# Performance work log

Measured on AMD Instinct MI355X. Metric: run time of the kernel, lower is better.

## Reference

```python
import jax, jax.numpy as jnp
import numpy as np
from jax import lax

B, S, H, T = 64, 512, 1024, 67


def setup_inputs() -> dict:
    key = jax.random.key(0)
    ks = jax.random.split(key, 8)
    hidden = jax.random.normal(ks[0], (B, S, H), jnp.float32)
    labels = jax.random.randint(ks[1], (B, S), 0, T)
    lengths = jax.random.randint(ks[2], (B,), S // 2, S + 1)
    mask = (jnp.arange(S)[None, :] < lengths[:, None]).astype(jnp.int32)  # prefix mask, mask[:,0]=1
    W = jax.random.normal(ks[3], (H, T), jnp.float32) * 0.02
    b = jnp.zeros((T,), jnp.float32)
    start_trans = jax.random.uniform(ks[4], (T,), jnp.float32, -0.1, 0.1)
    end_trans = jax.random.uniform(ks[5], (T,), jnp.float32, -0.1, 0.1)
    trans = jax.random.uniform(ks[6], (T, T), jnp.float32, -0.1, 0.1)
    return dict(hidden=hidden, labels=labels, mask=mask, W=W, b=b,
                start_trans=start_trans, end_trans=end_trans, trans=trans)


def _crf_llh(em, tags, mask, start_trans, end_trans, trans):
    # em: (B,S,T), tags: (B,S) int, mask: (B,S) bool. torchcrf log-likelihood per sequence.
    maskf = mask.astype(em.dtype)
    # numerator: score of the gold path
    em_tag = jnp.take_along_axis(em, tags[:, :, None], axis=2)[:, :, 0]       # (B,S)
    num = start_trans[tags[:, 0]] + em_tag[:, 0]
    trans_tag = trans[tags[:, :-1], tags[:, 1:]]                              # (B,S-1)
    num = num + jnp.sum((trans_tag + em_tag[:, 1:]) * maskf[:, 1:], axis=1)
    last_idx = jnp.sum(mask.astype(jnp.int32), axis=1) - 1                    # (B,)
    last_tags = jnp.take_along_axis(tags, last_idx[:, None], axis=1)[:, 0]
    num = num + end_trans[last_tags]
    # denominator: log partition via forward algorithm (scan over time)
    def step(score, x):
        em_i, m_i = x  # (B,T), (B,)
        nxt = jax.nn.logsumexp(score[:, :, None] + trans[None] + em_i[:, None, :], axis=1)
        return jnp.where(m_i[:, None], nxt, score), None
    init = start_trans[None, :] + em[:, 0]
    score, _ = lax.scan(step, init, (em[:, 1:].transpose(1, 0, 2), mask[:, 1:].T))
    denom = jax.nn.logsumexp(score + end_trans[None, :], axis=1)
    return num - denom


def _viterbi(em, mask, start_trans, end_trans, trans):
    # returns best tag sequence (B,S), padded positions set to 0
    n_tags = em.shape[-1]
    ident = jnp.arange(n_tags)[None, :]
    def fwd(score, x):
        em_i, m_i = x  # (B,T), (B,)
        cand = score[:, :, None] + trans[None]                                # (B,T,T)
        idx = jnp.argmax(cand, axis=1)                                        # (B,T)
        nxt = jnp.max(cand, axis=1) + em_i
        score = jnp.where(m_i[:, None], nxt, score)
        idx = jnp.where(m_i[:, None], idx, ident)  # identity link on padded steps
        return score, idx
    init = start_trans[None, :] + em[:, 0]
    score, hist = lax.scan(fwd, init, (em[:, 1:].transpose(1, 0, 2), mask[:, 1:].T))
    best = jnp.argmax(score + end_trans[None, :], axis=1)                     # (B,)
    def back(carry, h):  # carry = tag at t+1, h = hist[t]: (B,T)
        prev = jnp.take_along_axis(h, carry[:, None], axis=1)[:, 0]
        return prev, prev
    _, ys = lax.scan(back, best, hist, reverse=True)                          # (S-1,B) tags[0..S-2]
    tags = jnp.concatenate([ys.transpose(1, 0), best[:, None]], axis=1)       # (B,S)
    return jnp.where(mask, tags, 0)


def reference(hidden, labels, mask, W, b, start_trans, end_trans, trans):
    maskb = mask.astype(bool)
    # dropout is identity in eval mode
    em = jnp.einsum('bsh,ht->bst', jax.nn.leaky_relu(hidden, 0.01), W) + b     # token_scores
    llh = _crf_llh(em, labels, maskb, start_trans, end_trans, trans)
    loss = -jnp.sum(llh) / em.shape[0]
    tags = _viterbi(em, maskb, start_trans, end_trans, trans)
    return loss, tags, em
```

## Files before the change

kernel.cpp:

```cpp
#include <hip/hip_runtime.h>

#define Bn 64
#define Sn 512
#define Hn 1024
#define Tn 67

#define LOG2E 1.4426950408889634f
#define LN2   0.6931471805599453f

__global__ __launch_bounds__(256) void gemm_em(
    const float* __restrict__ hidden, const float* __restrict__ W,
    const float* __restrict__ bias, float* __restrict__ em,
    float* __restrict__ out)
{
    __shared__ __align__(16) float hs[64][36];
    __shared__ __align__(16) float wt[80][36];

    const int tid = threadIdx.x;
    const int tx = tid & 15, ty = tid >> 4;
    const int row0 = blockIdx.x * 64;

    if (blockIdx.x == 0 && tid == 0) out[0] = 0.0f;

    float acc[4][5];
#pragma unroll
    for (int u = 0; u < 4; ++u)
#pragma unroll
        for (int v = 0; v < 5; ++v) acc[u][v] = 0.f;

    for (int kc = 0; kc < Hn; kc += 32) {
#pragma unroll
        for (int l = 0; l < 2; ++l) {
            int idx = tid + l * 256;
            int r = idx >> 3, kq = (idx & 7) << 2;
            float4 v = *reinterpret_cast<const float4*>(
                &hidden[(size_t)(row0 + r) * Hn + kc + kq]);
            v.x = v.x > 0.f ? v.x : 0.01f * v.x;
            v.y = v.y > 0.f ? v.y : 0.01f * v.y;
            v.z = v.z > 0.f ? v.z : 0.01f * v.z;
            v.w = v.w > 0.f ? v.w : 0.01f * v.w;
            *reinterpret_cast<float4*>(&hs[r][kq]) = v;
        }
        for (int idx = tid; idx < 32 * Tn; idx += 256) {
            int k = idx / Tn;
            int t = idx - k * Tn;
            wt[t][k] = W[(size_t)(kc + k) * Tn + t];
        }
        __syncthreads();

#pragma unroll
        for (int k0 = 0; k0 < 32; k0 += 4) {
            float4 hv[4], wv[5];
#pragma unroll
            for (int u = 0; u < 4; ++u)
                hv[u] = *reinterpret_cast<float4*>(&hs[ty + 16 * u][k0]);
#pragma unroll
            for (int v = 0; v < 5; ++v)
                wv[v] = *reinterpret_cast<float4*>(&wt[tx + 16 * v][k0]);
#pragma unroll
            for (int u = 0; u < 4; ++u)
#pragma unroll
                for (int v = 0; v < 5; ++v) {
                    acc[u][v] = fmaf(hv[u].x, wv[v].x, acc[u][v]);
                    acc[u][v] = fmaf(hv[u].y, wv[v].y, acc[u][v]);
                    acc[u][v] = fmaf(hv[u].z, wv[v].z, acc[u][v]);
                    acc[u][v] = fmaf(hv[u].w, wv[v].w, acc[u][v]);
                }
        }
        __syncthreads();
    }

#pragma unroll
    for (int v = 0; v < 5; ++v) {
        int c = tx + 16 * v;
        if (c < Tn) {
            float bb = bias[c];
#pragma unroll
            for (int u = 0; u < 4; ++u) {
                int row = row0 + ty + 16 * u;
                em[(size_t)row * Tn + c] = acc[u][v] + bb;
            }
        }
    }
}

__global__ __launch_bounds__(128) void crf_scan(
    const float* __restrict__ em, const int* __restrict__ labels,
    const int* __restrict__ mask, const float* __restrict__ startT,
    const float* __restrict__ endT, const float* __restrict__ trans,
    float* __restrict__ out)
{
    __shared__ __align__(16) float sArr[68];
    __shared__ __align__(16) float pArr[68];
    __shared__ float redf[128];
    __shared__ int   redi[128];
    __shared__ unsigned char hist[Sn - 1][68];
    __shared__ int tg[Sn];

    const int tid = threadIdx.x;
    const bool isV = blockIdx.x >= 64;
    const int b = blockIdx.x & 63;
    const int j = tid;
    const bool act = j < Tn;
    const int jj = act ? j : 0;
    const float* emb = em + (size_t)b * Sn * Tn;
    const int* maskb = mask + b * Sn;

    if (tid == 67) { sArr[67] = -1e30f; pArr[67] = 0.f; }

    if (!isV) {
        float Ecol[68];
#pragma unroll
        for (int i = 0; i < Tn; ++i)
            Ecol[i] = exp2f(trans[i * Tn + jj] * LOG2E);
        Ecol[67] = 0.f;

        float sc = act ? (startT[jj] + emb[jj]) : -1e30f;
        if (act) sArr[j] = sc;
        __syncthreads();

        float em_cur = act ? emb[(size_t)Tn + jj] : 0.f;
        int m_cur = maskb[1];

        for (int t = 1; t < Sn; ++t) {
            float em_nxt = 0.f; int m_nxt = 0;
            if (t + 1 < Sn) {
                em_nxt = act ? emb[(size_t)(t + 1) * Tn + jj] : 0.f;
                m_nxt = maskb[t + 1];
            }
            float mx = -1e30f;
#pragma unroll
            for (int i4 = 0; i4 < 17; ++i4) {
                float4 v = *reinterpret_cast<float4*>(&sArr[4 * i4]);
                mx = fmaxf(mx, fmaxf(fmaxf(v.x, v.y), fmaxf(v.z, v.w)));
            }
            float p = act ? exp2f((sc - mx) * LOG2E) : 0.f;
            if (act) pArr[j] = p;
            __syncthreads();
            float a0 = 0.f, a1 = 0.f, a2 = 0.f, a3 = 0.f;
#pragma unroll
            for (int i4 = 0; i4 < 17; ++i4) {
                float4 pv = *reinterpret_cast<float4*>(&pArr[4 * i4]);
                a0 = fmaf(pv.x, Ecol[4 * i4 + 0], a0);
                a1 = fmaf(pv.y, Ecol[4 * i4 + 1], a1);
                a2 = fmaf(pv.z, Ecol[4 * i4 + 2], a2);
                a3 = fmaf(pv.w, Ecol[4 * i4 + 3], a3);
            }
            float ssum = (a0 + a1) + (a2 + a3);
            float nxt = mx + log2f(ssum) * LN2 + em_cur;
            if (m_cur) sc = nxt;
            if (act) sArr[j] = sc;
            __syncthreads();
            em_cur = em_nxt; m_cur = m_nxt;
        }

        float v = act ? (sc + endT[jj]) : -1e30f;
        if (act) sArr[j] = v;
        __syncthreads();
        float mx = -1e30f;
#pragma unroll
        for (int i4 = 0; i4 < 17; ++i4) {
            float4 sv = *reinterpret_cast<float4*>(&sArr[4 * i4]);
            mx = fmaxf(mx, fmaxf(fmaxf(sv.x, sv.y), fmaxf(sv.z, sv.w)));
        }
        float p = act ? exp2f((v - mx) * LOG2E) : 0.f;
        if (act) pArr[j] = p;
        __syncthreads();
        float s0 = 0.f;
#pragma unroll
        for (int i4 = 0; i4 < 17; ++i4) {
            float4 pv = *reinterpret_cast<float4*>(&pArr[4 * i4]);
            s0 += (pv.x + pv.y) + (pv.z + pv.w);
        }
        float denom = mx + log2f(s0) * LN2;

        float part = 0.f; int lenp = 0;
        for (int s = tid; s < Sn; s += 128) {
            int ms = maskb[s];
            lenp += ms;
            int ls = labels[b * Sn + s];
            if (s == 0) {
                part += startT[ls] + emb[ls];
            } else if (ms) {
                int lp = labels[b * Sn + s - 1];
                part += trans[lp * Tn + ls] + emb[(size_t)s * Tn + ls];
            }
        }
        redf[tid] = part; redi[tid] = lenp;
        __syncthreads();
        if (tid == 0) {
            float num = 0.f; int len = 0;
            for (int i = 0; i < 128; ++i) { num += redf[i]; len += redi[i]; }
            int last = labels[b * Sn + len - 1];
            num += endT[last];
            float llh = num - denom;
            atomicAdd(out, -llh * (1.0f / (float)Bn));
        }
    } else {
        float Tcol[68];
#pragma unroll
        for (int i = 0; i < Tn; ++i) Tcol[i] = trans[i * Tn + jj];
        Tcol[67] = 0.f;

        float sc = act ? (startT[jj] + emb[jj]) : -1e30f;
        if (act) sArr[j] = sc;
        __syncthreads();

        float em_cur = act ? emb[(size_t)Tn + jj] : 0.f;
        int m_cur = maskb[1];

        for (int t = 1; t < Sn; ++t) {
            float em_nxt = 0.f; int m_nxt = 0;
            if (t + 1 < Sn) {
                em_nxt = act ? emb[(size_t)(t + 1) * Tn + jj] : 0.f;
                m_nxt = maskb[t + 1];
            }
            float best = -1e30f; int bi = 0;
#pragma unroll
            for (int i4 = 0; i4 < 17; ++i4) {
                float4 sv = *reinterpret_cast<float4*>(&sArr[4 * i4]);
                float c0 = sv.x + Tcol[4 * i4 + 0];
                if (c0 > best) { best = c0; bi = 4 * i4 + 0; }
                float c1 = sv.y + Tcol[4 * i4 + 1];
                if (c1 > best) { best = c1; bi = 4 * i4 + 1; }
                float c2 = sv.z + Tcol[4 * i4 + 2];
                if (c2 > best) { best = c2; bi = 4 * i4 + 2; }
                float c3 = sv.w + Tcol[4 * i4 + 3];
                if (c3 > best) { best = c3; bi = 4 * i4 + 3; }
            }
            float nxt = best + em_cur;
            int idx = m_cur ? bi : j;
            if (m_cur) sc = nxt;
            __syncthreads();
            if (act) { hist[t - 1][j] = (unsigned char)idx; sArr[j] = sc; }
            __syncthreads();
            em_cur = em_nxt; m_cur = m_nxt;
        }

        float v = act ? (sc + endT[jj]) : -1e30f;
        if (act) pArr[j] = v;
        __syncthreads();
        if (tid == 0) {
            float best = -1e30f; int bi = 0;
            for (int i = 0; i < Tn; ++i) {
                float c = pArr[i];
                if (c > best) { best = c; bi = i; }
            }
            int carry = bi;
            tg[Sn - 1] = carry;
            for (int k = Sn - 2; k >= 0; --k) {
                carry = hist[k][carry];
                tg[k] = carry;
            }
        }
        __syncthreads();
        float* tagsOut = out + 1 + b * Sn;
        for (int s = tid; s < Sn; s += 128)
            tagsOut[s] = maskb[s] ? (float)tg[s] : 0.f;
    }
}

extern "C" void kernel_launch(void* const* d_in, const int* in_sizes, int n_in,
                              void* d_out, int out_size, void* d_ws, size_t ws_size,
                              hipStream_t stream) {
    const float* hidden = (const float*)d_in[0];
    const int*   labels = (const int*)d_in[1];
    const int*   maskp  = (const int*)d_in[2];
    const float* W      = (const float*)d_in[3];
    const float* bias   = (const float*)d_in[4];
    const float* startT = (const float*)d_in[5];
    const float* endT   = (const float*)d_in[6];
    const float* trans  = (const float*)d_in[7];
    float* out = (float*)d_out;
    float* em  = out + 1 + (size_t)Bn * Sn;

    hipLaunchKernelGGL(gemm_em, dim3((Bn * Sn) / 64), dim3(256), 0, stream,
                       hidden, W, bias, em, out);
    hipLaunchKernelGGL(crf_scan, dim3(128), dim3(128), 0, stream,
                       em, labels, maskp, startT, endT, trans, out);
}
```

Baseline: 849.2 us.

## Fuse CRF forward and Viterbi into one block, staging emissions in LDS

Forward and Viterbi scans for a batch row now run in one 256-thread block, two waves each, instead of separate blocks. Emissions are double-buffered in shared memory in 32-step chunks so the serial loop avoids global loads. The forward pass shifts by the previous step's tag-0 score instead of recomputing a max, which drops one barrier per step. Viterbi uses a tree argmax. Risks: the stale shift could lose numerical stability, and each branch calls its own barrier inside the loop, relying on matching counts across divergent waves.

```diff
diff --git a/kernel.cpp b/kernel.cpp
--- a/kernel.cpp
+++ b/kernel.cpp
@@ -84,180 +84,211 @@
     }
 }
 
-__global__ __launch_bounds__(128) void crf_scan(
+__global__ __launch_bounds__(256) void crf_scan2(
     const float* __restrict__ em, const int* __restrict__ labels,
     const int* __restrict__ mask, const float* __restrict__ startT,
     const float* __restrict__ endT, const float* __restrict__ trans,
     float* __restrict__ out)
 {
-    __shared__ __align__(16) float sArr[68];
-    __shared__ __align__(16) float pArr[68];
-    __shared__ float redf[128];
-    __shared__ int   redi[128];
+    __shared__ __align__(16) float pbuf[2][72];
+    __shared__ __align__(16) float vbuf[2][72];
+    __shared__ __align__(16) float em_lds[2][32 * Tn];
+    __shared__ int mask_lds[Sn];
     __shared__ unsigned char hist[Sn - 1][68];
     __shared__ int tg[Sn];
+    __shared__ float redf[256];
+    __shared__ int redi[256];
 
     const int tid = threadIdx.x;
-    const bool isV = blockIdx.x >= 64;
-    const int b = blockIdx.x & 63;
-    const int j = tid;
-    const bool act = j < Tn;
-    const int jj = act ? j : 0;
-    const float* emb = em + (size_t)b * Sn * Tn;
-    const int* maskb = mask + b * Sn;
-
-    if (tid == 67) { sArr[67] = -1e30f; pArr[67] = 0.f; }
-
-    if (!isV) {
+    const int wid = tid >> 6;
+    const int lane = tid & 63;
+    const int b = blockIdx.x;
+    const bool isCRF = wid < 2;
+    const bool hiw = (wid & 1);
+    const int st = hiw ? (64 + (lane < 3 ? lane : 2)) : lane;
+    const bool active = (!hiw) || (lane < 3);
+    const float* emg = em + (size_t)b * Sn * Tn;
+
+    for (int i = tid; i < 32 * Tn; i += 256) em_lds[0][i] = emg[i];
+    for (int i = tid; i < Sn; i += 256) mask_lds[i] = mask[b * Sn + i];
+    if (tid == 0) {
+        pbuf[0][67] = 0.f; pbuf[1][67] = 0.f;
+        vbuf[0][67] = -1e30f; vbuf[1][67] = -1e30f;
+    }
+    __syncthreads();
+
+    float sc = startT[st] + em_lds[0][st];
+    if (isCRF) { if (active) pbuf[1][st] = sc; }
+    else       { if (active) vbuf[0][st] = sc; }
+    __syncthreads();
+    if (isCRF) {
+        float M0 = pbuf[1][0];
+        float p = exp2f((sc - M0) * LOG2E);
+        if (active) pbuf[0][st] = p;
+        if (tid == 0) { pbuf[0][68] = sc; pbuf[0][69] = M0; }
+    }
+    __syncthreads();
+
+    int bufc = 0;
+    if (isCRF) {
         float Ecol[68];
 #pragma unroll
-        for (int i = 0; i < Tn; ++i)
-            Ecol[i] = exp2f(trans[i * Tn + jj] * LOG2E);
+        for (int i = 0; i < Tn; ++i) Ecol[i] = exp2f(trans[i * Tn + st] * LOG2E);
         Ecol[67] = 0.f;
 
-        float sc = act ? (startT[jj] + emb[jj]) : -1e30f;
-        if (act) sArr[j] = sc;
-        __syncthreads();
-
-        float em_cur = act ? emb[(size_t)Tn + jj] : 0.f;
-        int m_cur = maskb[1];
-
         for (int t = 1; t < Sn; ++t) {
-            float em_nxt = 0.f; int m_nxt = 0;
-            if (t + 1 < Sn) {
-                em_nxt = act ? emb[(size_t)(t + 1) * Tn + jj] : 0.f;
-                m_nxt = maskb[t + 1];
-            }
-            float mx = -1e30f;
-#pragma unroll
-            for (int i4 = 0; i4 < 17; ++i4) {
-                float4 v = *reinterpret_cast<float4*>(&sArr[4 * i4]);
-                mx = fmaxf(mx, fmaxf(fmaxf(v.x, v.y), fmaxf(v.z, v.w)));
-            }
-            float p = act ? exp2f((sc - mx) * LOG2E) : 0.f;
-            if (act) pArr[j] = p;
+            if ((t & 31) == 1) {
+                int k = (t >> 5) + 1;
+                if (k < 16) {
+                    const float* src = emg + (size_t)k * 32 * Tn;
+                    float* dst = em_lds[k & 1];
+                    for (int i = tid; i < 32 * Tn; i += 128) dst[i] = src[i];
+                }
+            }
+            const float* row = em_lds[(t >> 5) & 1] + (t & 31) * Tn;
+            float em_t = row[st];
+            int m = mask_lds[t];
+            float M_used = pbuf[bufc][69];
+            float sc0p   = pbuf[bufc][68];
+            const float4* P = (const float4*)&pbuf[bufc][0];
+            float a0 = 0.f, a1 = 0.f, a2 = 0.f, a3 = 0.f;
+#pragma unroll
+            for (int q = 0; q < 17; ++q) {
+                float4 pv = P[q];
+                a0 = fmaf(pv.x, Ecol[4 * q + 0], a0);
+                a1 = fmaf(pv.y, Ecol[4 * q + 1], a1);
+                a2 = fmaf(pv.z, Ecol[4 * q + 2], a2);
+                a3 = fmaf(pv.w, Ecol[4 * q + 3], a3);
+            }
+            float aa = (a0 + a1) + (a2 + a3);
+            float nxt = M_used + log2f(aa) * LN2 + em_t;
+            if (m) sc = nxt;
+            float Mn = sc0p;
+            float p = exp2f((sc - Mn) * LOG2E);
+            int nb = bufc ^ 1;
+            if (active) pbuf[nb][st] = p;
+            if (tid == 0) { pbuf[nb][68] = sc; pbuf[nb][69] = Mn; }
             __syncthreads();
-            float a0 = 0.f, a1 = 0.f, a2 = 0.f, a3 = 0.f;
-#pragma unroll
-            for (int i4 = 0; i4 < 17; ++i4) {
-                float4 pv = *reinterpret_cast<float4*>(&pArr[4 * i4]);
-                a0 = fmaf(pv.x, Ecol[4 * i4 + 0], a0);
-                a1 = fmaf(pv.y, Ecol[4 * i4 + 1], a1);
-                a2 = fmaf(pv.z, Ecol[4 * i4 + 2], a2);
-                a3 = fmaf(pv.w, Ecol[4 * i4 + 3], a3);
-            }
-            float ssum = (a0 + a1) + (a2 + a3);
-            float nxt = mx + log2f(ssum) * LN2 + em_cur;
-            if (m_cur) sc = nxt;
-            if (act) sArr[j] = sc;
-            __syncthreads();
-            em_cur = em_nxt; m_cur = m_nxt;
-        }
-
-        float v = act ? (sc + endT[jj]) : -1e30f;
-        if (act) sArr[j] = v;
-        __syncthreads();
-        float mx = -1e30f;
-#pragma unroll
-        for (int i4 = 0; i4 < 17; ++i4) {
-            float4 sv = *reinterpret_cast<float4*>(&sArr[4 * i4]);
-            mx = fmaxf(mx, fmaxf(fmaxf(sv.x, sv.y), fmaxf(sv.z, sv.w)));
-        }
-        float p = act ? exp2f((v - mx) * LOG2E) : 0.f;
-        if (act) pArr[j] = p;
-        __syncthreads();
-        float s0 = 0.f;
-#pragma unroll
-        for (int i4 = 0; i4 < 17; ++i4) {
-            float4 pv = *reinterpret_cast<float4*>(&pArr[4 * i4]);
-            s0 += (pv.x + pv.y) + (pv.z + pv.w);
-        }
-        float denom = mx + log2f(s0) * LN2;
-
-        float part = 0.f; int lenp = 0;
-        for (int s = tid; s < Sn; s += 128) {
-            int ms = maskb[s];
-            lenp += ms;
-            int ls = labels[b * Sn + s];
-            if (s == 0) {
-                part += startT[ls] + emb[ls];
-            } else if (ms) {
-                int lp = labels[b * Sn + s - 1];
-                part += trans[lp * Tn + ls] + emb[(size_t)s * Tn + ls];
-            }
-        }
-        redf[tid] = part; redi[tid] = lenp;
-        __syncthreads();
-        if (tid == 0) {
-            float num = 0.f; int len = 0;
-            for (int i = 0; i < 128; ++i) { num += redf[i]; len += redi[i]; }
-            int last = labels[b * Sn + len - 1];
-            num += endT[last];
-            float llh = num - denom;
-            atomicAdd(out, -llh * (1.0f / (float)Bn));
+            bufc = nb;
         }
     } else {
         float Tcol[68];
 #pragma unroll
-        for (int i = 0; i < Tn; ++i) Tcol[i] = trans[i * Tn + jj];
+        for (int i = 0; i < Tn; ++i) Tcol[i] = trans[i * Tn + st];
         Tcol[67] = 0.f;
 
-        float sc = act ? (startT[jj] + emb[jj]) : -1e30f;
-        if (act) sArr[j] = sc;
-        __syncthreads();
-
-        float em_cur = act ? emb[(size_t)Tn + jj] : 0.f;
-        int m_cur = maskb[1];
-
         for (int t = 1; t < Sn; ++t) {
-            float em_nxt = 0.f; int m_nxt = 0;
-            if (t + 1 < Sn) {
-                em_nxt = act ? emb[(size_t)(t + 1) * Tn + jj] : 0.f;
-                m_nxt = maskb[t + 1];
-            }
-            float best = -1e30f; int bi = 0;
-#pragma unroll
-            for (int i4 = 0; i4 < 17; ++i4) {
-                float4 sv = *reinterpret_cast<float4*>(&sArr[4 * i4]);
-                float c0 = sv.x + Tcol[4 * i4 + 0];
-                if (c0 > best) { best = c0; bi = 4 * i4 + 0; }
-                float c1 = sv.y + Tcol[4 * i4 + 1];
-                if (c1 > best) { best = c1; bi = 4 * i4 + 1; }
-                float c2 = sv.z + Tcol[4 * i4 + 2];
-                if (c2 > best) { best = c2; bi = 4 * i4 + 2; }
-                float c3 = sv.w + Tcol[4 * i4 + 3];
-                if (c3 > best) { best = c3; bi = 4 * i4 + 3; }
-            }
-            float nxt = best + em_cur;
-            int idx = m_cur ? bi : j;
-            if (m_cur) sc = nxt;
+            const float* row = em_lds[(t >> 5) & 1] + (t & 31) * Tn;
+            float em_t = row[st];
+            int m = mask_lds[t];
+            const float4* Vp = (const float4*)&vbuf[bufc][0];
+            float bvv[34]; int bx[34];
+#pragma unroll
+            for (int q = 0; q < 17; ++q) {
+                float4 v = Vp[q];
+                float c0 = v.x + Tcol[4 * q + 0];
+                float c1 = v.y + Tcol[4 * q + 1];
+                float c2 = v.z + Tcol[4 * q + 2];
+                float c3 = v.w + Tcol[4 * q + 3];
+                bool r0 = c1 > c0;
+                bvv[2 * q]     = r0 ? c1 : c0;
+                bx[2 * q]      = r0 ? 4 * q + 1 : 4 * q + 0;
+                bool r1 = c3 > c2;
+                bvv[2 * q + 1] = r1 ? c3 : c2;
+                bx[2 * q + 1]  = r1 ? 4 * q + 3 : 4 * q + 2;
+            }
+#pragma unroll
+            for (int q = 0; q < 17; ++q) {
+                bool r = bvv[2 * q + 1] > bvv[2 * q];
+                bvv[q] = r ? bvv[2 * q + 1] : bvv[2 * q];
+                bx[q]  = r ? bx[2 * q + 1]  : bx[2 * q];
+            }
+#pragma unroll
+            for (int q = 0; q < 8; ++q) {
+                bool r = bvv[2 * q + 1] > bvv[2 * q];
+                bvv[q] = r ? bvv[2 * q + 1] : bvv[2 * q];
+                bx[q]  = r ? bx[2 * q + 1]  : bx[2 * q];
+            }
+            bvv[8] = bvv[16]; bx[8] = bx[16];
+#pragma unroll
+            for (int q = 0; q < 4; ++q) {
+                bool r = bvv[2 * q + 1] > bvv[2 * q];
+                bvv[q] = r ? bvv[2 * q + 1] : bvv[2 * q];
+                bx[q]  = r ? bx[2 * q + 1]  : bx[2 * q];
+            }
+            bvv[4] = bvv[8]; bx[4] = bx[8];
+#pragma unroll
+            for (int q = 0; q < 2; ++q) {
+                bool r = bvv[2 * q + 1] > bvv[2 * q];
+                bvv[q] = r ? bvv[2 * q + 1] : bvv[2 * q];
+                bx[q]  = r ? bx[2 * q + 1]  : bx[2 * q];
+            }
+            bvv[2] = bvv[4]; bx[2] = bx[4];
+            { bool r = bvv[1] > bvv[0]; bvv[0] = r ? bvv[1] : bvv[0]; bx[0] = r ? bx[1] : bx[0]; }
+            { bool r = bvv[2] > bvv[0]; bvv[0] = r ? bvv[2] : bvv[0]; bx[0] = r ? bx[2] : bx[0]; }
+
+            float nv = bvv[0] + em_t;
+            int idx = m ? bx[0] : st;
+            if (m) sc = nv;
+            int nb = bufc ^ 1;
+            if (active) {
+                hist[t - 1][st] = (unsigned char)idx;
+                vbuf[nb][st] = sc;
+            }
             __syncthreads();
-            if (act) { hist[t - 1][j] = (unsigned char)idx; sArr[j] = sc; }
-            __syncthreads();
-            em_cur = em_nxt; m_cur = m_nxt;
-        }
-
-        float v = act ? (sc + endT[jj]) : -1e30f;
-        if (act) pArr[j] = v;
-        __syncthreads();
-        if (tid == 0) {
-            float best = -1e30f; int bi = 0;
-            for (int i = 0; i < Tn; ++i) {
-                float c = pArr[i];
-                if (c > best) { best = c; bi = i; }
-            }
-            int carry = bi;
-            tg[Sn - 1] = carry;
-            for (int k = Sn - 2; k >= 0; --k) {
-                carry = hist[k][carry];
-                tg[k] = carry;
-            }
-        }
-        __syncthreads();
-        float* tagsOut = out + 1 + b * Sn;
-        for (int s = tid; s < Sn; s += 128)
-            tagsOut[s] = maskb[s] ? (float)tg[s] : 0.f;
-    }
+            bufc = nb;
+        }
+    }
+
+    if (isCRF) { if (active) pbuf[0][st] = sc + endT[st]; }
+    else       { if (active) vbuf[0][st] = sc + endT[st]; }
+    __syncthreads();
+
+    float part = 0.f; int lenp = 0;
+    for (int s = tid; s < Sn; s += 256) {
+        int ms = mask_lds[s];
+        lenp += ms;
+        int ls = labels[b * Sn + s];
+        if (s == 0) {
+            part += startT[ls] + emg[ls];
+        } else if (ms) {
+            int lp = labels[b * Sn + s - 1];
+            part += trans[lp * Tn + ls] + emg[(size_t)s * Tn + ls];
+        }
+    }
+    redf[tid] = part; redi[tid] = lenp;
+    __syncthreads();
+
+    if (tid == 0) {
+        float mx = -1e30f;
+        for (int i = 0; i < Tn; ++i) mx = fmaxf(mx, pbuf[0][i]);
+        float ss = 0.f;
+        for (int i = 0; i < Tn; ++i) ss += exp2f((pbuf[0][i] - mx) * LOG2E);
+        float denom = mx + log2f(ss) * LN2;
+        float num = 0.f; int len = 0;
+        for (int i = 0; i < 256; ++i) { num += redf[i]; len += redi[i]; }
+        int last = labels[b * Sn + len - 1];
+        num += endT[last];
+        atomicAdd(out, -(num - denom) * (1.0f / (float)Bn));
+    }
+    if (tid == 128) {
+        float best = -1e30f; int bi = 0;
+        for (int i = 0; i < Tn; ++i) {
+            float c = vbuf[0][i];
+            if (c > best) { best = c; bi = i; }
+        }
+        int carry = bi;
+        tg[Sn - 1] = carry;
+        for (int k = Sn - 2; k >= 0; --k) {
+            carry = hist[k][carry];
+            tg[k] = carry;
+        }
+    }
+    __syncthreads();
+
+    float* tagsOut = out + 1 + b * Sn;
+    for (int s = tid; s < Sn; s += 256)
+        tagsOut[s] = mask_lds[s] ? (float)tg[s] : 0.f;
 }
 
 extern "C" void kernel_launch(void* const* d_in, const int* in_sizes, int n_in,
@@ -276,6 +307,6 @@
 
     hipLaunchKernelGGL(gemm_em, dim3((Bn * Sn) / 64), dim3(256), 0, stream,
                        hidden, W, bias, em, out);
-    hipLaunchKernelGGL(crf_scan, dim3(128), dim3(128), 0, stream,
+    hipLaunchKernelGGL(crf_scan2, dim3(Bn), dim3(256), 0, stream,
                        em, labels, maskp, startT, endT, trans, out);
 }
```

New measurement: 712.7 us. 16.1% less time.

## Run CRF forward and Viterbi scans as single-wavefront warps without block barriers

Applied to the files above, without the earlier changes.

The CRF scan is restructured so each batch row gets one block of three wavefronts: one runs the forward logsumexp recursion, one runs Viterbi, and one computes the gold-path numerator. Each recursion lives inside a single 64-lane wavefront, with each lane owning one or two tags, double-buffered LDS vectors and wave shuffles/ballots in place of the per-step __syncthreads barriers. The transition matrix (exp'd for forward) is staged in shared memory in a float4-transposed layout instead of per-thread registers. The forward pass also reuses the previous step's lane-0 score as the max shift rather than doing a full max reduction, which relies on scores staying in a safe range.

```diff
diff --git a/kernel.cpp b/kernel.cpp
--- a/kernel.cpp
+++ b/kernel.cpp
@@ -84,179 +84,272 @@
     }
 }
 
-__global__ __launch_bounds__(128) void crf_scan(
+#define R17(X) X(0) X(1) X(2) X(3) X(4) X(5) X(6) X(7) X(8) X(9) X(10) X(11) X(12) X(13) X(14) X(15) X(16)
+
+__global__ __launch_bounds__(192, 1) void crf_scan7(
     const float* __restrict__ em, const int* __restrict__ labels,
     const int* __restrict__ mask, const float* __restrict__ startT,
     const float* __restrict__ endT, const float* __restrict__ trans,
     float* __restrict__ out)
 {
-    __shared__ __align__(16) float sArr[68];
-    __shared__ __align__(16) float pArr[68];
-    __shared__ float redf[128];
-    __shared__ int   redi[128];
+    __shared__ __align__(16) float4 EcT4[17 * 68];
+    __shared__ __align__(16) float4 TcT4[17 * 68];
+    __shared__ __align__(16) float pb[2][72];
+    __shared__ __align__(16) float vb[2][72];
+    __shared__ int maskC[Sn];
+    __shared__ int maskV[Sn];
     __shared__ unsigned char hist[Sn - 1][68];
     __shared__ int tg[Sn];
+    __shared__ float numSh;
+    __shared__ int lenSh;
 
     const int tid = threadIdx.x;
-    const bool isV = blockIdx.x >= 64;
-    const int b = blockIdx.x & 63;
-    const int j = tid;
-    const bool act = j < Tn;
-    const int jj = act ? j : 0;
-    const float* emb = em + (size_t)b * Sn * Tn;
-    const int* maskb = mask + b * Sn;
-
-    if (tid == 67) { sArr[67] = -1e30f; pArr[67] = 0.f; }
-
-    if (!isV) {
-        float Ecol[68];
-#pragma unroll
-        for (int i = 0; i < Tn; ++i)
-            Ecol[i] = exp2f(trans[i * Tn + jj] * LOG2E);
-        Ecol[67] = 0.f;
-
-        float sc = act ? (startT[jj] + emb[jj]) : -1e30f;
-        if (act) sArr[j] = sc;
-        __syncthreads();
-
-        float em_cur = act ? emb[(size_t)Tn + jj] : 0.f;
-        int m_cur = maskb[1];
+    const int wid = tid >> 6;
+    const int lane = tid & 63;
+    const int b = blockIdx.x;
+    const float* emg = em + (size_t)b * Sn * Tn;
+    const int u2 = lane < 3 ? lane : 2;
+    const int st2 = 64 + u2;
+
+    if (wid == 0) {
+#pragma unroll
+        for (int i = 0; i < 8; ++i)
+            maskC[lane + i * 64] = mask[b * Sn + lane + i * 64];
+
+        for (int idx = lane; idx < 17 * 68; idx += 64) {
+            int i4 = idx / 68, j = idx - i4 * 68;
+            int i0 = 4 * i4;
+            float4 e;
+            e.x = (i0 + 0 < Tn && j < Tn) ? exp2f(trans[(i0 + 0) * Tn + j] * LOG2E) : 0.f;
+            e.y = (i0 + 1 < Tn && j < Tn) ? exp2f(trans[(i0 + 1) * Tn + j] * LOG2E) : 0.f;
+            e.z = (i0 + 2 < Tn && j < Tn) ? exp2f(trans[(i0 + 2) * Tn + j] * LOG2E) : 0.f;
+            e.w = (i0 + 3 < Tn && j < Tn) ? exp2f(trans[(i0 + 3) * Tn + j] * LOG2E) : 0.f;
+            EcT4[idx] = e;
+        }
+        if (lane == 0) { pb[0][67] = 0.f; pb[1][67] = 0.f; }
+
+        float em0a = emg[lane];
+        float em0b = emg[st2];
+        float sc1 = startT[lane] + em0a;
+        float sc2 = startT[st2] + em0b;
+        float M = __shfl(sc1, 0);
+        float p1 = exp2f((sc1 - M) * LOG2E);
+        float p2 = exp2f((sc2 - M) * LOG2E);
+        pb[0][lane] = p1;
+        if (lane < 3) pb[0][64 + lane] = p2;
+        float Mprev = M;
+
+        float emn1 = emg[Tn + lane];
+        float emn2 = emg[Tn + st2];
+        int mn = maskC[1];
 
         for (int t = 1; t < Sn; ++t) {
-            float em_nxt = 0.f; int m_nxt = 0;
+            float emc1 = emn1, emc2 = emn2;
+            int m = mn;
             if (t + 1 < Sn) {
-                em_nxt = act ? emb[(size_t)(t + 1) * Tn + jj] : 0.f;
-                m_nxt = maskb[t + 1];
-            }
-            float mx = -1e30f;
-#pragma unroll
-            for (int i4 = 0; i4 < 17; ++i4) {
-                float4 v = *reinterpret_cast<float4*>(&sArr[4 * i4]);
-                mx = fmaxf(mx, fmaxf(fmaxf(v.x, v.y), fmaxf(v.z, v.w)));
-            }
-            float p = act ? exp2f((sc - mx) * LOG2E) : 0.f;
-            if (act) pArr[j] = p;
-            __syncthreads();
-            float a0 = 0.f, a1 = 0.f, a2 = 0.f, a3 = 0.f;
-#pragma unroll
-            for (int i4 = 0; i4 < 17; ++i4) {
-                float4 pv = *reinterpret_cast<float4*>(&pArr[4 * i4]);
-                a0 = fmaf(pv.x, Ecol[4 * i4 + 0], a0);
-                a1 = fmaf(pv.y, Ecol[4 * i4 + 1], a1);
-                a2 = fmaf(pv.z, Ecol[4 * i4 + 2], a2);
-                a3 = fmaf(pv.w, Ecol[4 * i4 + 3], a3);
-            }
-            float ssum = (a0 + a1) + (a2 + a3);
-            float nxt = mx + log2f(ssum) * LN2 + em_cur;
-            if (m_cur) sc = nxt;
-            if (act) sArr[j] = sc;
-            __syncthreads();
-            em_cur = em_nxt; m_cur = m_nxt;
-        }
-
-        float v = act ? (sc + endT[jj]) : -1e30f;
-        if (act) sArr[j] = v;
-        __syncthreads();
+                emn1 = emg[(size_t)(t + 1) * Tn + lane];
+                emn2 = emg[(size_t)(t + 1) * Tn + st2];
+                mn = maskC[t + 1];
+            }
+            const float4* P = (const float4*)&pb[(t + 1) & 1][0];
+            float a0 = 0, a1 = 0, a2 = 0, a3 = 0;
+            float g0 = 0, g1 = 0, g2 = 0, g3 = 0;
+#pragma unroll
+            for (int q = 0; q < 17; ++q) {
+                float4 pv = P[q];
+                float4 e1 = EcT4[q * 68 + lane];
+                float4 e2 = EcT4[q * 68 + 64 + u2];
+                a0 = fmaf(pv.x, e1.x, a0); g0 = fmaf(pv.x, e2.x, g0);
+                a1 = fmaf(pv.y, e1.y, a1); g1 = fmaf(pv.y, e2.y, g1);
+                a2 = fmaf(pv.z, e1.z, a2); g2 = fmaf(pv.z, e2.z, g2);
+                a3 = fmaf(pv.w, e1.w, a3); g3 = fmaf(pv.w, e2.w, g3);
+            }
+            float s1 = (a0 + a1) + (a2 + a3);
+            float s2 = (g0 + g1) + (g2 + g3);
+            float n1 = Mprev + log2f(s1) * LN2 + emc1;
+            float n2 = Mprev + log2f(s2) * LN2 + emc2;
+            if (m) { sc1 = n1; sc2 = n2; }
+            M = __shfl(sc1, 0);
+            p1 = exp2f((sc1 - M) * LOG2E);
+            p2 = exp2f((sc2 - M) * LOG2E);
+            float* Wp = &pb[t & 1][0];
+            Wp[lane] = p1;
+            if (lane < 3) Wp[64 + lane] = p2;
+            Mprev = M;
+        }
+
+        float* F = &pb[0][0];
+        F[lane] = sc1 + endT[lane];
+        if (lane < 3) F[64 + lane] = sc2 + endT[64 + lane];
+        if (lane == 0) F[67] = -1e30f;
         float mx = -1e30f;
-#pragma unroll
-        for (int i4 = 0; i4 < 17; ++i4) {
-            float4 sv = *reinterpret_cast<float4*>(&sArr[4 * i4]);
-            mx = fmaxf(mx, fmaxf(fmaxf(sv.x, sv.y), fmaxf(sv.z, sv.w)));
-        }
-        float p = act ? exp2f((v - mx) * LOG2E) : 0.f;
-        if (act) pArr[j] = p;
-        __syncthreads();
-        float s0 = 0.f;
-#pragma unroll
-        for (int i4 = 0; i4 < 17; ++i4) {
-            float4 pv = *reinterpret_cast<float4*>(&pArr[4 * i4]);
-            s0 += (pv.x + pv.y) + (pv.z + pv.w);
-        }
-        float denom = mx + log2f(s0) * LN2;
-
-        float part = 0.f; int lenp = 0;
-        for (int s = tid; s < Sn; s += 128) {
-            int ms = maskb[s];
-            lenp += ms;
-            int ls = labels[b * Sn + s];
-            if (s == 0) {
-                part += startT[ls] + emb[ls];
-            } else if (ms) {
-                int lp = labels[b * Sn + s - 1];
-                part += trans[lp * Tn + ls] + emb[(size_t)s * Tn + ls];
-            }
-        }
-        redf[tid] = part; redi[tid] = lenp;
-        __syncthreads();
-        if (tid == 0) {
-            float num = 0.f; int len = 0;
-            for (int i = 0; i < 128; ++i) { num += redf[i]; len += redi[i]; }
-            int last = labels[b * Sn + len - 1];
-            num += endT[last];
-            float llh = num - denom;
-            atomicAdd(out, -llh * (1.0f / (float)Bn));
-        }
-    } else {
-        float Tcol[68];
-#pragma unroll
-        for (int i = 0; i < Tn; ++i) Tcol[i] = trans[i * Tn + jj];
-        Tcol[67] = 0.f;
-
-        float sc = act ? (startT[jj] + emb[jj]) : -1e30f;
-        if (act) sArr[j] = sc;
-        __syncthreads();
-
-        float em_cur = act ? emb[(size_t)Tn + jj] : 0.f;
-        int m_cur = maskb[1];
+        const float4* Fv = (const float4*)F;
+#pragma unroll
+        for (int q = 0; q < 17; ++q) {
+            float4 v = Fv[q];
+            mx = fmaxf(mx, fmaxf(fmaxf(v.x, v.y), fmaxf(v.z, v.w)));
+        }
+        float ss = 0.f;
+#pragma unroll
+        for (int q = 0; q < 17; ++q) {
+            float4 v = Fv[q];
+            ss += exp2f((v.x - mx) * LOG2E) + exp2f((v.y - mx) * LOG2E)
+                + exp2f((v.z - mx) * LOG2E) + exp2f((v.w - mx) * LOG2E);
+        }
+        float denom = mx + log2f(ss) * LN2;
+        __syncthreads();
+        if (lane == 0) {
+            int len = lenSh;
+            float num = numSh + endT[labels[b * Sn + len - 1]];
+            atomicAdd(out, -(num - denom) * (1.0f / (float)Bn));
+        }
+    } else if (wid == 1) {
+#pragma unroll
+        for (int i = 0; i < 8; ++i)
+            maskV[lane + i * 64] = mask[b * Sn + lane + i * 64];
+
+        for (int idx = lane; idx < 17 * 68; idx += 64) {
+            int i4 = idx / 68, j = idx - i4 * 68;
+            int i0 = 4 * i4;
+            float4 e;
+            e.x = (i0 + 0 < Tn && j < Tn) ? trans[(i0 + 0) * Tn + j] : 0.f;
+            e.y = (i0 + 1 < Tn && j < Tn) ? trans[(i0 + 1) * Tn + j] : 0.f;
+            e.z = (i0 + 2 < Tn && j < Tn) ? trans[(i0 + 2) * Tn + j] : 0.f;
+            e.w = (i0 + 3 < Tn && j < Tn) ? trans[(i0 + 3) * Tn + j] : 0.f;
+            TcT4[idx] = e;
+        }
+        const int rsec = (lane < 3) ? (64 + lane) : 0;
+        float Tsf0 = trans[lane * Tn + 64], Tsf1 = trans[lane * Tn + 65], Tsf2 = trans[lane * Tn + 66];
+        float Tss0 = trans[rsec * Tn + 64], Tss1 = trans[rsec * Tn + 65], Tss2 = trans[rsec * Tn + 66];
+
+        if (lane == 0) { vb[0][67] = -1e30f; vb[1][67] = -1e30f; }
+
+        float em0a = emg[lane];
+        float em0b = emg[st2];
+        float sc1 = startT[lane] + em0a;
+        float sc2 = startT[st2] + em0b;
+        vb[0][lane] = sc1;
+        if (lane < 3) vb[0][64 + lane] = sc2;
+
+        float emn1 = emg[Tn + lane];
+        float emn2 = emg[Tn + st2];
+        int mn = maskV[1];
 
         for (int t = 1; t < Sn; ++t) {
-            float em_nxt = 0.f; int m_nxt = 0;
+            float emc1 = emn1, emc2 = emn2;
+            int m = mn;
             if (t + 1 < Sn) {
-                em_nxt = act ? emb[(size_t)(t + 1) * Tn + jj] : 0.f;
-                m_nxt = maskb[t + 1];
-            }
-            float best = -1e30f; int bi = 0;
-#pragma unroll
-            for (int i4 = 0; i4 < 17; ++i4) {
-                float4 sv = *reinterpret_cast<float4*>(&sArr[4 * i4]);
-                float c0 = sv.x + Tcol[4 * i4 + 0];
-                if (c0 > best) { best = c0; bi = 4 * i4 + 0; }
-                float c1 = sv.y + Tcol[4 * i4 + 1];
-                if (c1 > best) { best = c1; bi = 4 * i4 + 1; }
-                float c2 = sv.z + Tcol[4 * i4 + 2];
-                if (c2 > best) { best = c2; bi = 4 * i4 + 2; }
-                float c3 = sv.w + Tcol[4 * i4 + 3];
-                if (c3 > best) { best = c3; bi = 4 * i4 + 3; }
-            }
-            float nxt = best + em_cur;
-            int idx = m_cur ? bi : j;
-            if (m_cur) sc = nxt;
-            __syncthreads();
-            if (act) { hist[t - 1][j] = (unsigned char)idx; sArr[j] = sc; }
-            __syncthreads();
-            em_cur = em_nxt; m_cur = m_nxt;
-        }
-
-        float v = act ? (sc + endT[jj]) : -1e30f;
-        if (act) pArr[j] = v;
-        __syncthreads();
-        if (tid == 0) {
-            float best = -1e30f; int bi = 0;
-            for (int i = 0; i < Tn; ++i) {
-                float c = pArr[i];
-                if (c > best) { best = c; bi = i; }
-            }
-            int carry = bi;
+                emn1 = emg[(size_t)(t + 1) * Tn + lane];
+                emn2 = emg[(size_t)(t + 1) * Tn + st2];
+                mn = maskV[t + 1];
+            }
+            const float4* Vbc = (const float4*)&vb[(t + 1) & 1][0];
+
+            float x0 = sc1 + Tsf0, x1 = sc1 + Tsf1, x2 = sc1 + Tsf2;
+            float y0 = sc2 + Tss0, y1 = sc2 + Tss1, y2 = sc2 + Tss2;
+            float z0 = (lane < 3) ? fmaxf(x0, y0) : x0;
+            float z1 = (lane < 3) ? fmaxf(x1, y1) : x1;
+            float z2 = (lane < 3) ? fmaxf(x2, y2) : x2;
+#pragma unroll
+            for (int k = 1; k < 64; k <<= 1) {
+                z0 = fmaxf(z0, __shfl_xor(z0, k));
+                z1 = fmaxf(z1, __shfl_xor(z1, k));
+                z2 = fmaxf(z2, __shfl_xor(z2, k));
+            }
+            unsigned long long ba0 = __ballot(x0 == z0);
+            unsigned long long ba1 = __ballot(x1 == z1);
+            unsigned long long ba2 = __ballot(x2 == z2);
+            unsigned long long bb0 = __ballot((lane < 3) && (y0 == z0));
+            unsigned long long bb1 = __ballot((lane < 3) && (y1 == z1));
+            unsigned long long bb2 = __ballot((lane < 3) && (y2 == z2));
+            int e0 = ba0 ? (__ffsll(ba0) - 1) : (64 + __ffsll(bb0) - 1);
+            int e1 = ba1 ? (__ffsll(ba1) - 1) : (64 + __ffsll(bb1) - 1);
+            int e2 = ba2 ? (__ffsll(ba2) - 1) : (64 + __ffsll(bb2) - 1);
+
+#define VDECL(i) float4 c##i; { float4 v = Vbc[i]; float4 tt = TcT4[i * 68 + lane]; \
+            c##i.x = v.x + tt.x; c##i.y = v.y + tt.y; c##i.z = v.z + tt.z; c##i.w = v.w + tt.w; }
+            R17(VDECL)
+#undef VDECL
+#define VQM(i) float mq##i = fmaxf(fmaxf(c##i.x, c##i.y), fmaxf(c##i.z, c##i.w));
+            R17(VQM)
+#undef VQM
+            float m1 = fmaxf(
+                fmaxf(fmaxf(fmaxf(mq0, mq1), fmaxf(mq2, mq3)),
+                      fmaxf(fmaxf(mq4, mq5), fmaxf(mq6, mq7))),
+                fmaxf(fmaxf(fmaxf(mq8, mq9), fmaxf(mq10, mq11)),
+                      fmaxf(fmaxf(mq12, mq13), fmaxf(fmaxf(mq14, mq15), mq16))));
+#define VIQ(i) int sel##i = (mq##i == m1) ? (4 * i + (c##i.x == mq##i ? 0 : (c##i.y == mq##i ? 1 : (c##i.z == mq##i ? 2 : 3)))) : 1023;
+            R17(VIQ)
+#undef VIQ
+            int idxp = min(
+                min(min(min(sel0, sel1), min(sel2, sel3)),
+                    min(min(sel4, sel5), min(sel6, sel7))),
+                min(min(min(sel8, sel9), min(sel10, sel11)),
+                    min(min(sel12, sel13), min(min(sel14, sel15), sel16))));
+
+            float n1 = m1 + emc1;
+            float nuv = ((u2 == 0) ? z0 : (u2 == 1) ? z1 : z2) + emc2;
+            int nui = (u2 == 0) ? e0 : (u2 == 1) ? e1 : e2;
+
+            int idx1 = m ? idxp : lane;
+            int idx2 = m ? nui : st2;
+            if (m) { sc1 = n1; sc2 = nuv; }
+
+            hist[t - 1][lane] = (unsigned char)idx1;
+            float* Wv = &vb[t & 1][0];
+            Wv[lane] = sc1;
+            if (lane < 3) {
+                hist[t - 1][64 + lane] = (unsigned char)idx2;
+                Wv[64 + lane] = sc2;
+            }
+        }
+
+        float f1 = sc1 + endT[lane];
+        float f2 = (lane < 3) ? (sc2 + endT[64 + lane]) : -1e30f;
+        float zf = fmaxf(f1, f2);
+#pragma unroll
+        for (int k = 1; k < 64; k <<= 1) zf = fmaxf(zf, __shfl_xor(zf, k));
+        unsigned long long bf1 = __ballot(f1 == zf);
+        unsigned long long bf2 = __ballot((lane < 3) && (f2 == zf));
+        int best = bf1 ? (__ffsll(bf1) - 1) : (64 + __ffsll(bf2) - 1);
+
+        if (lane == 0) {
+            int carry = best;
             tg[Sn - 1] = carry;
             for (int k = Sn - 2; k >= 0; --k) {
                 carry = hist[k][carry];
                 tg[k] = carry;
             }
         }
-        __syncthreads();
         float* tagsOut = out + 1 + b * Sn;
-        for (int s = tid; s < Sn; s += 128)
-            tagsOut[s] = maskb[s] ? (float)tg[s] : 0.f;
+#pragma unroll
+        for (int i = 0; i < 8; ++i) {
+            int s = lane + i * 64;
+            tagsOut[s] = maskV[s] ? (float)tg[s] : 0.f;
+        }
+        __syncthreads();
+    } else {
+        float part = 0.f; int lenp = 0;
+#pragma unroll
+        for (int i = 0; i < 8; ++i) {
+            int s = lane + i * 64;
+            int ms = mask[b * Sn + s];
+            lenp += ms;
+            int ls = labels[b * Sn + s];
+            if (s == 0) {
+                part += startT[ls] + emg[ls];
+            } else if (ms) {
+                int lp = labels[b * Sn + s - 1];
+                part += trans[lp * Tn + ls] + emg[(size_t)s * Tn + ls];
+            }
+        }
+#pragma unroll
+        for (int k = 1; k < 64; k <<= 1) {
+            part += __shfl_xor(part, k);
+            lenp += __shfl_xor(lenp, k);
+        }
+        if (lane == 0) { numSh = part; lenSh = lenp; }
+        __syncthreads();
     }
 }
 
@@ -276,6 +369,6 @@
 
     hipLaunchKernelGGL(gemm_em, dim3((Bn * Sn) / 64), dim3(256), 0, stream,
                        hidden, W, bias, em, out);
-    hipLaunchKernelGGL(crf_scan, dim3(128), dim3(128), 0, stream,
+    hipLaunchKernelGGL(crf_scan7, dim3(Bn), dim3(192), 0, stream,
                        em, labels, maskp, startT, endT, trans, out);
 }
```

Result: slower. 893.1 us (+5.2%).
